# Performance work log

Hardware: AMD Instinct MI355X
Metric: run time of the kernel (lower is better)

The kernel has to match this reference:

```python
import jax, jax.numpy as jnp
import numpy as np

N_NODES = 100000
N_EDGES = 1600000
IN_DIM = 128
OUT_DIM = 64


def setup_inputs() -> dict:
    key = jax.random.key(0)
    k1, k2, k3 = jax.random.split(key, 3)
    x = jax.random.normal(k1, (N_NODES, IN_DIM), dtype=jnp.float32)
    edge_index = jax.random.randint(k2, (2, N_EDGES), 0, N_NODES, dtype=jnp.int64)
    W = jax.random.normal(k3, (IN_DIM, OUT_DIM), dtype=jnp.float32) * (1.0 / np.sqrt(IN_DIM))
    b = jnp.zeros((OUT_DIM,), dtype=jnp.float32)
    return {"x": x, "edge_index": edge_index, "W": W, "b": b}


def reference(x, edge_index, W, b):
    row = edge_index[0]  # source nodes
    col = edge_index[1]  # target nodes (aggregation index)
    n = x.shape[0]

    # gcn_norm with add_self_loops=False: degree from edge weights (ones) at target
    ones = jnp.ones((edge_index.shape[1],), dtype=x.dtype)
    deg = jax.ops.segment_sum(ones, col, num_segments=n)  # [N]
    deg_inv_sqrt = jnp.where(deg > 0, jax.lax.rsqrt(jnp.maximum(deg, 1e-12)), 0.0)
    norm = deg_inv_sqrt[row] * deg_inv_sqrt[col]  # [E]

    # linear transform first (bias added after aggregation, as in PyG GCNConv)
    h = x @ W  # [N, OUT_DIM]

    # gather source features, scale by norm, scatter-add to targets
    msg = h[row] * norm[:, None]  # [E, OUT_DIM]
    out = jax.ops.segment_sum(msg, col, num_segments=n) + b  # [N, OUT_DIM]

    return jax.nn.relu(out)
```

## Files before the change

kernel.cpp:

```cpp
#include <hip/hip_runtime.h>
#include <hip/hip_bf16.h>

#define IN_DIM 128
#define OUT_DIM 64
#define FLOG 7
#define FNPB (1 << FLOG)
#define MAXFINE 1024
#define BB 512
#define BT 512
#define MAXE 8
#define NGRP 8
#define CAP_G 512
#define CAP (NGRP * CAP_G)
#define SPILL_MAX 65536
#define KFT 256
#define HALF 64
#define SBUF_CAP 2048

static inline size_t align_up(size_t v, size_t a) { return (v + a - 1) & ~(a - 1); }

__device__ __forceinline__ unsigned short f2bf(float f) {
    unsigned int x = __float_as_uint(f);
    unsigned int r = (x + 0x7fffu + ((x >> 16) & 1u)) >> 16;
    return (unsigned short)r;
}

typedef _Float16 half8 __attribute__((ext_vector_type(8)));
typedef float f32x4 __attribute__((ext_vector_type(4)));

__global__ void __launch_bounds__(BT, 4) k_build_mm(
    const int* __restrict__ row, const int* __restrict__ col,
    int* __restrict__ BinSize, unsigned int* __restrict__ EdgeBuf,
    uint2* __restrict__ spill, int* __restrict__ spillcur,
    const float* __restrict__ x, const float* __restrict__ W,
    unsigned short* __restrict__ h,
    int n_edges, int n_nodes, int nbf, int chunk, int mm_blocks) {
    if ((int)blockIdx.x < BB) {
        __shared__ int hist[MAXFINE];
        int t = threadIdx.x;
        int g = blockIdx.x & (NGRP - 1);
        int start = blockIdx.x * chunk;
        int end = min(n_edges, start + chunk);
        int n = end - start;

        for (int i = t; i < nbf; i += BT) hist[i] = 0;
        __syncthreads();

        int er[MAXE], ec[MAXE];
#pragma unroll
        for (int u = 0; u < MAXE; ++u) {
            int i = t + u * BT;
            ec[u] = -1;
            if (i < n) {
                er[u] = row[start + i];
                int c = col[start + i];
                ec[u] = c;
                atomicAdd(&hist[c >> FLOG], 1);
            }
        }
        __syncthreads();
        for (int i = t; i < nbf; i += BT) {
            int cv = hist[i];
            hist[i] = cv ? atomicAdd(&BinSize[g * nbf + i], cv) : 0;
        }
        __syncthreads();
#pragma unroll
        for (int u = 0; u < MAXE; ++u) {
            int c = ec[u];
            if (c >= 0) {
                int bin = c >> FLOG;
                int pos = atomicAdd(&hist[bin], 1);
                if (pos < CAP_G) {
                    EdgeBuf[(size_t)bin * CAP + g * CAP_G + pos] =
                        ((unsigned int)er[u] << FLOG) | (unsigned int)(c & (FNPB - 1));
                } else {
                    int sp = atomicAdd(spillcur, 1);
                    if (sp < SPILL_MAX)
                        spill[sp] = make_uint2((unsigned int)er[u], (unsigned int)c);
                }
            }
        }
    } else {
        const int lane = threadIdx.x & 63;
        const int m = lane & 15;
        const int q = lane >> 4;
        const int wv = threadIdx.x >> 6;
        const int wid0 = ((int)blockIdx.x - BB) * 8 + wv;
        const int nwaves = mm_blocks * 8;
        const int ntiles = (n_nodes + 15) >> 4;

        half8 bfrag[4][4];
#pragma unroll
        for (int kt = 0; kt < 4; ++kt) {
#pragma unroll
            for (int nt = 0; nt < 4; ++nt) {
                int k0 = kt * 32 + q * 8;
                int c = nt * 16 + m;
#pragma unroll
                for (int j = 0; j < 8; ++j)
                    bfrag[kt][nt][j] = (_Float16)W[(size_t)(k0 + j) * OUT_DIM + c];
            }
        }

        for (int wid = wid0; wid < ntiles; wid += nwaves) {
            const int nb = wid << 4;
            int arow = nb + m;
            if (arow >= n_nodes) arow = n_nodes - 1;
            const float* xr = x + (size_t)arow * IN_DIM;

            f32x4 acc[4];
#pragma unroll
            for (int nt = 0; nt < 4; ++nt) acc[nt] = (f32x4){0.f, 0.f, 0.f, 0.f};

#pragma unroll
            for (int kt = 0; kt < 4; ++kt) {
                const float4* xp = (const float4*)(xr + kt * 32 + q * 8);
                float4 lo = xp[0];
                float4 hi = xp[1];
                half8 afrag;
                afrag[0] = (_Float16)lo.x; afrag[1] = (_Float16)lo.y;
                afrag[2] = (_Float16)lo.z; afrag[3] = (_Float16)lo.w;
                afrag[4] = (_Float16)hi.x; afrag[5] = (_Float16)hi.y;
                afrag[6] = (_Float16)hi.z; afrag[7] = (_Float16)hi.w;
#pragma unroll
                for (int nt = 0; nt < 4; ++nt)
                    acc[nt] = __builtin_amdgcn_mfma_f32_16x16x32_f16(
                        afrag, bfrag[kt][nt], acc[nt], 0, 0, 0);
            }

#pragma unroll
            for (int r = 0; r < 4; ++r) {
                int node = nb + q * 4 + r;
                if (node < n_nodes) {
                    unsigned short* hp = h + (size_t)node * OUT_DIM + m;
#pragma unroll
                    for (int nt = 0; nt < 4; ++nt)
                        hp[nt * 16] = f2bf(acc[nt][r]);
                }
            }
        }
    }
}

__global__ void __launch_bounds__(256) kD_degree(
    const unsigned int* __restrict__ EdgeBuf, const int* __restrict__ BinSize,
    const uint2* __restrict__ spill, const int* __restrict__ spillcur,
    float* __restrict__ dis, int* __restrict__ cntg, int n_nodes, int nbf) {
    __shared__ int cnt[FNPB];
    int t = threadIdx.x;
    int b = blockIdx.x;
    if (t < FNPB) cnt[t] = 0;
    __syncthreads();
    for (int g = 0; g < NGRP; ++g) {
        int szg = min(BinSize[g * nbf + b], CAP_G);
        const unsigned int* sl = EdgeBuf + (size_t)b * CAP + g * CAP_G;
        for (int i = t; i < szg; i += 256)
            atomicAdd(&cnt[sl[i] & (FNPB - 1)], 1);
    }
    int sn = min(*spillcur, SPILL_MAX);
    for (int i = t; i < sn; i += 256) {
        uint2 e = spill[i];
        if ((int)(e.y >> FLOG) == b) atomicAdd(&cnt[e.y & (FNPB - 1)], 1);
    }
    __syncthreads();
    if (t < FNPB) {
        int d = cnt[t];
        cntg[(size_t)b * FNPB + t] = d;
        int node = (b << FLOG) + t;
        if (node < n_nodes)
            dis[node] = (d > 0) ? rsqrtf((float)d) : 0.0f;
    }
}

__global__ void __launch_bounds__(KFT) kF_sortagg(
    const unsigned int* __restrict__ EdgeBuf, const int* __restrict__ BinSize,
    const uint2* __restrict__ spill, const int* __restrict__ spillcur,
    const unsigned short* __restrict__ h, const float* __restrict__ dis,
    const int* __restrict__ cntg, const float* __restrict__ b,
    float* __restrict__ out, int* __restrict__ arena, int* __restrict__ arenacur,
    int n_nodes, int nbf) {
    __shared__ int cnt[HALF];
    __shared__ int seg[HALF];
    __shared__ int cursor[HALF];
    __shared__ int sbuf[SBUF_CAP];
    __shared__ int abase_sh;
    int t = threadIdx.x;
    int bk = blockIdx.x >> 1;
    int halfid = blockIdx.x & 1;
    int lo = halfid * HALF;
    int nb0 = (bk << FLOG) + lo;
    int sn = min(*spillcur, SPILL_MAX);

    if (t < 64) {
        int c = cntg[(size_t)bk * FNPB + lo + t];
        int s = c;
#pragma unroll
        for (int off = 1; off < 64; off <<= 1) {
            int y = __shfl_up(s, off, 64);
            if (t >= off) s += y;
        }
        cnt[t] = c;
        seg[t] = s;
        cursor[t] = s - c;
    }
    __syncthreads();

    int ne = seg[HALF - 1];
    if (t == 0 && ne > SBUF_CAP) abase_sh = atomicAdd(arenacur, ne);
    __syncthreads();

    const int lane = t & 63;
    const int wv = t >> 6;
    const int quarter = lane >> 4;
    const int qlane = lane & 15;
    float4 bias = ((const float4*)b)[qlane];

    if (ne <= SBUF_CAP) {
        for (int g = 0; g < NGRP; ++g) {
            int szg = min(BinSize[g * nbf + bk], CAP_G);
            const unsigned int* sl = EdgeBuf + (size_t)bk * CAP + g * CAP_G;
            for (int i = t; i < szg; i += KFT) {
                unsigned int v = sl[i];
                int nlocal = (int)(v & (FNPB - 1)) - lo;
                if ((unsigned)nlocal < HALF) {
                    int p = atomicAdd(&cursor[nlocal], 1);
                    sbuf[p] = (int)(v >> FLOG);
                }
            }
        }
        for (int i = t; i < sn; i += KFT) {
            uint2 e = spill[i];
            if ((int)(e.y >> FLOG) == bk) {
                int nlocal = (int)(e.y & (FNPB - 1)) - lo;
                if ((unsigned)nlocal < HALF) {
                    int p = atomicAdd(&cursor[nlocal], 1);
                    sbuf[p] = (int)e.x;
                }
            }
        }
        __syncthreads();

        for (int nl = wv; nl < HALF; nl += 4) {
            int node = nb0 + nl;
            if (node >= n_nodes) break;
            int e_ = seg[nl];
            int dcount = cnt[nl];
            int s_ = e_ - dcount;
            float a0 = 0.f, a1 = 0.f, a2 = 0.f, a3 = 0.f;
            for (int j0 = s_; j0 < e_; j0 += 16) {
                int i0 = j0 + quarter;
                int i1 = i0 + 4;
                int i2 = i0 + 8;
                int i3 = i0 + 12;
                int r0 = sbuf[i0 < e_ ? i0 : s_];
                int r1 = sbuf[i1 < e_ ? i1 : s_];
                int r2 = sbuf[i2 < e_ ? i2 : s_];
                int r3 = sbuf[i3 < e_ ? i3 : s_];
                float d0 = dis[r0];
                float d1 = dis[r1];
                float d2 = dis[r2];
                float d3 = dis[r3];
                uint2 v0 = make_uint2(0u, 0u), v1 = v0, v2 = v0, v3 = v0;
                if (i0 < e_)
                    v0 = *(const uint2*)(h + (size_t)r0 * OUT_DIM + qlane * 4);
                if (i1 < e_)
                    v1 = *(const uint2*)(h + (size_t)r1 * OUT_DIM + qlane * 4);
                if (i2 < e_)
                    v2 = *(const uint2*)(h + (size_t)r2 * OUT_DIM + qlane * 4);
                if (i3 < e_)
                    v3 = *(const uint2*)(h + (size_t)r3 * OUT_DIM + qlane * 4);
                a0 = fmaf(__uint_as_float(v0.x << 16), d0, a0);
                a1 = fmaf(__uint_as_float(v0.x & 0xFFFF0000u), d0, a1);
                a2 = fmaf(__uint_as_float(v0.y << 16), d0, a2);
                a3 = fmaf(__uint_as_float(v0.y & 0xFFFF0000u), d0, a3);
                a0 = fmaf(__uint_as_float(v1.x << 16), d1, a0);
                a1 = fmaf(__uint_as_float(v1.x & 0xFFFF0000u), d1, a1);
                a2 = fmaf(__uint_as_float(v1.y << 16), d1, a2);
                a3 = fmaf(__uint_as_float(v1.y & 0xFFFF0000u), d1, a3);
                a0 = fmaf(__uint_as_float(v2.x << 16), d2, a0);
                a1 = fmaf(__uint_as_float(v2.x & 0xFFFF0000u), d2, a1);
                a2 = fmaf(__uint_as_float(v2.y << 16), d2, a2);
                a3 = fmaf(__uint_as_float(v2.y & 0xFFFF0000u), d2, a3);
                a0 = fmaf(__uint_as_float(v3.x << 16), d3, a0);
                a1 = fmaf(__uint_as_float(v3.x & 0xFFFF0000u), d3, a1);
                a2 = fmaf(__uint_as_float(v3.y << 16), d3, a2);
                a3 = fmaf(__uint_as_float(v3.y & 0xFFFF0000u), d3, a3);
            }
            a0 += __shfl_xor(a0, 16, 64); a0 += __shfl_xor(a0, 32, 64);
            a1 += __shfl_xor(a1, 16, 64); a1 += __shfl_xor(a1, 32, 64);
            a2 += __shfl_xor(a2, 16, 64); a2 += __shfl_xor(a2, 32, 64);
            a3 += __shfl_xor(a3, 16, 64); a3 += __shfl_xor(a3, 32, 64);
            if (quarter == 0) {
                float dv = (dcount > 0) ? rsqrtf((float)dcount) : 0.0f;
                float4 o;
                o.x = fmaxf(fmaf(a0, dv, bias.x), 0.f);
                o.y = fmaxf(fmaf(a1, dv, bias.y), 0.f);
                o.z = fmaxf(fmaf(a2, dv, bias.z), 0.f);
                o.w = fmaxf(fmaf(a3, dv, bias.w), 0.f);
                ((float4*)(out + (size_t)node * OUT_DIM))[qlane] = o;
            }
        }
    } else {
        int abase = abase_sh;
        for (int g = 0; g < NGRP; ++g) {
            int szg = min(BinSize[g * nbf + bk], CAP_G);
            const unsigned int* sl = EdgeBuf + (size_t)bk * CAP + g * CAP_G;
            for (int i = t; i < szg; i += KFT) {
                unsigned int v = sl[i];
                int nlocal = (int)(v & (FNPB - 1)) - lo;
                if ((unsigned)nlocal < HALF) {
                    int p = atomicAdd(&cursor[nlocal], 1);
                    arena[abase + p] = (int)(v >> FLOG);
                }
            }
        }
        for (int i = t; i < sn; i += KFT) {
            uint2 e = spill[i];
            if ((int)(e.y >> FLOG) == bk) {
                int nlocal = (int)(e.y & (FNPB - 1)) - lo;
                if ((unsigned)nlocal < HALF) {
                    int p = atomicAdd(&cursor[nlocal], 1);
                    arena[abase + p] = (int)e.x;
                }
            }
        }
        __threadfence();
        __syncthreads();
        for (int nl = wv; nl < HALF; nl += 4) {
            int node = nb0 + nl;
            if (node >= n_nodes) break;
            int e_ = seg[nl];
            int dcount = cnt[nl];
            int s_ = e_ - dcount;
            float a0 = 0.f, a1 = 0.f, a2 = 0.f, a3 = 0.f;
            for (int j0 = s_; j0 < e_; j0 += 8) {
                int iA = j0 + quarter;
                int iB = j0 + quarter + 4;
                int rA = arena[abase + (iA < e_ ? iA : s_)];
                int rB = arena[abase + (iB < e_ ? iB : s_)];
                float dA = dis[rA];
                float dB = dis[rB];
                uint2 vA = make_uint2(0u, 0u), vB = make_uint2(0u, 0u);
                if (iA < e_)
                    vA = *(const uint2*)(h + (size_t)rA * OUT_DIM + qlane * 4);
                if (iB < e_)
                    vB = *(const uint2*)(h + (size_t)rB * OUT_DIM + qlane * 4);
                a0 = fmaf(__uint_as_float(vA.x << 16), dA, a0);
                a1 = fmaf(__uint_as_float(vA.x & 0xFFFF0000u), dA, a1);
                a2 = fmaf(__uint_as_float(vA.y << 16), dA, a2);
                a3 = fmaf(__uint_as_float(vA.y & 0xFFFF0000u), dA, a3);
                a0 = fmaf(__uint_as_float(vB.x << 16), dB, a0);
                a1 = fmaf(__uint_as_float(vB.x & 0xFFFF0000u), dB, a1);
                a2 = fmaf(__uint_as_float(vB.y << 16), dB, a2);
                a3 = fmaf(__uint_as_float(vB.y & 0xFFFF0000u), dB, a3);
            }
            a0 += __shfl_xor(a0, 16, 64); a0 += __shfl_xor(a0, 32, 64);
            a1 += __shfl_xor(a1, 16, 64); a1 += __shfl_xor(a1, 32, 64);
            a2 += __shfl_xor(a2, 16, 64); a2 += __shfl_xor(a2, 32, 64);
            a3 += __shfl_xor(a3, 16, 64); a3 += __shfl_xor(a3, 32, 64);
            if (quarter == 0) {
                float dv = (dcount > 0) ? rsqrtf((float)dcount) : 0.0f;
                float4 o;
                o.x = fmaxf(fmaf(a0, dv, bias.x), 0.f);
                o.y = fmaxf(fmaf(a1, dv, bias.y), 0.f);
                o.z = fmaxf(fmaf(a2, dv, bias.z), 0.f);
                o.w = fmaxf(fmaf(a3, dv, bias.w), 0.f);
                ((float4*)(out + (size_t)node * OUT_DIM))[qlane] = o;
            }
        }
    }
}

#define MM_NODES 16
__global__ void __launch_bounds__(256) k_matmul_f32(
    const float* __restrict__ x, const float* __restrict__ W,
    const float* __restrict__ dis, float* __restrict__ h, int n_nodes) {
    __shared__ float xs[MM_NODES * IN_DIM];
    const int lane = threadIdx.x & 63;
    const int wv = threadIdx.x >> 6;
    float w[IN_DIM];
#pragma unroll
    for (int k = 0; k < IN_DIM; ++k) w[k] = W[k * OUT_DIM + lane];
    int nchunks = (n_nodes + MM_NODES - 1) / MM_NODES;
    for (int ch = blockIdx.x; ch < nchunks; ch += gridDim.x) {
        int base = ch * MM_NODES;
        int nrows = min(MM_NODES, n_nodes - base);
        __syncthreads();
        const float4* xg = (const float4*)(x + (size_t)base * IN_DIM);
        int nf4 = nrows * IN_DIM / 4;
        for (int i = threadIdx.x; i < nf4; i += 256) ((float4*)xs)[i] = xg[i];
        __syncthreads();
#pragma unroll
        for (int j = 0; j < 4; ++j) {
            int local = wv * 4 + j;
            int node = base + local;
            if (local < nrows) {
                const float4* xr = (const float4*)(xs + local * IN_DIM);
                float acc = 0.0f;
#pragma unroll
                for (int k4 = 0; k4 < IN_DIM / 4; ++k4) {
                    float4 xv = xr[k4];
                    acc = fmaf(xv.x, w[k4 * 4 + 0], acc);
                    acc = fmaf(xv.y, w[k4 * 4 + 1], acc);
                    acc = fmaf(xv.z, w[k4 * 4 + 2], acc);
                    acc = fmaf(xv.w, w[k4 * 4 + 3], acc);
                }
                h[(size_t)node * OUT_DIM + lane] = acc * dis[node];
            }
        }
    }
}

__global__ void k_degree_fb(const int* __restrict__ col, int* __restrict__ deg,
                            int n_edges) {
    int i = blockIdx.x * blockDim.x + threadIdx.x;
    int stride = gridDim.x * blockDim.x;
    for (; i < n_edges; i += stride) atomicAdd(&deg[col[i]], 1);
}

__global__ void k_rsqrt_fb(const int* __restrict__ deg, float* __restrict__ dis, int n) {
    int i = blockIdx.x * blockDim.x + threadIdx.x;
    if (i < n) {
        int d = deg[i];
        dis[i] = (d > 0) ? rsqrtf((float)d) : 0.0f;
    }
}

__global__ void __launch_bounds__(256) k_scatter_fb(
    const int* __restrict__ row, const int* __restrict__ col,
    const float* __restrict__ dis, const float* __restrict__ h,
    float* __restrict__ out, int n_edges) {
    const int lane = threadIdx.x & 63;
    int e = (blockIdx.x * blockDim.x + threadIdx.x) >> 6;
    int nw = (gridDim.x * blockDim.x) >> 6;
    for (; e < n_edges; e += nw) {
        int r = row[e];
        int c = col[e];
        float v = h[(size_t)r * OUT_DIM + lane] * dis[c];
        atomicAdd(&out[(size_t)c * OUT_DIM + lane], v);
    }
}

__global__ void k_bias_relu_fb(float* __restrict__ out, const float* __restrict__ b,
                               int total) {
    int i = blockIdx.x * blockDim.x + threadIdx.x;
    int stride = gridDim.x * blockDim.x;
    for (; i < total; i += stride) {
        float v = out[i] + b[i & (OUT_DIM - 1)];
        out[i] = fmaxf(v, 0.0f);
    }
}

extern "C" void kernel_launch(void* const* d_in, const int* in_sizes, int n_in,
                              void* d_out, int out_size, void* d_ws, size_t ws_size,
                              hipStream_t stream) {
    const float* x = (const float*)d_in[0];
    const int* ei = (const int*)d_in[1];
    const float* W = (const float*)d_in[2];
    const float* b = (const float*)d_in[3];
    float* out = (float*)d_out;

    const int n_nodes = in_sizes[0] / IN_DIM;
    const int n_edges = in_sizes[1] / 2;
    const int* row = ei;
    const int* col = ei + n_edges;

    const int nbf = (n_nodes + FNPB - 1) >> FLOG;
    const int chunk = (n_edges + BB - 1) / BB;

    char* wsb = (char*)d_ws;
    size_t off = 0;
    int* BinSize = (int*)(wsb + off);    off += (size_t)(nbf * NGRP + 8) * 4;
    int* spillcur = BinSize + nbf * NGRP;
    int* arenacur = BinSize + nbf * NGRP + 1;
    const size_t zero_bytes = off;
    off = align_up(off, 256);
    unsigned int* EdgeBuf = (unsigned int*)(wsb + off);
                                         off += align_up((size_t)nbf * CAP * 4, 256);
    uint2* spill = (uint2*)(wsb + off);  off += align_up((size_t)SPILL_MAX * 8, 256);
    int* arena = (int*)(wsb + off);      off += align_up((size_t)n_edges * 4, 256);
    float* dis = (float*)(wsb + off);    off += align_up((size_t)n_nodes * 4, 256);
    int* cntg = (int*)(wsb + off);       off += align_up((size_t)nbf * FNPB * 4, 256);
    unsigned short* h = (unsigned short*)(wsb + off);
                                         off += (size_t)n_nodes * OUT_DIM * 2;
    const size_t needed = off;

    const bool ok = (ws_size >= needed) && (nbf <= MAXFINE) &&
                    (chunk <= MAXE * BT) && (n_nodes <= (1 << 24));

    if (ok) {
        const int ntiles = (n_nodes + 15) >> 4;
        int mm_blocks = (ntiles + 15) / 16;
        if (mm_blocks < 1) mm_blocks = 1;
        hipMemsetAsync(BinSize, 0, zero_bytes, stream);
        k_build_mm<<<BB + mm_blocks, BT, 0, stream>>>(
            row, col, BinSize, EdgeBuf, spill, spillcur,
            x, W, h, n_edges, n_nodes, nbf, chunk, mm_blocks);
        kD_degree<<<nbf, 256, 0, stream>>>(EdgeBuf, BinSize, spill, spillcur,
                                           dis, cntg, n_nodes, nbf);
        kF_sortagg<<<2 * nbf, KFT, 0, stream>>>(EdgeBuf, BinSize, spill, spillcur,
                                                h, dis, cntg, b, out, arena,
                                                arenacur, n_nodes, nbf);
    } else {
        char* p = (char*)d_ws;
        int* deg_f = (int*)p;
        float* dis_f = (float*)(p + align_up((size_t)n_nodes * 4, 256));
        float* h_f = (float*)(p + 2 * align_up((size_t)n_nodes * 4, 256));
        hipMemsetAsync(deg_f, 0, (size_t)n_nodes * 4, stream);
        hipMemsetAsync(out, 0, (size_t)out_size * 4, stream);
        k_degree_fb<<<1024, 256, 0, stream>>>(col, deg_f, n_edges);
        k_rsqrt_fb<<<(n_nodes + 255) / 256, 256, 0, stream>>>(deg_f, dis_f, n_nodes);
        k_matmul_f32<<<1024, 256, 0, stream>>>(x, W, dis_f, h_f, n_nodes);
        k_scatter_fb<<<2048, 256, 0, stream>>>(row, col, dis_f, h_f, out, n_edges);
        k_bias_relu_fb<<<2048, 256, 0, stream>>>(out, b, n_nodes * OUT_DIM);
    }
}
```

Before: 172.2 us.

## Stage edges in LDS by bin before coalesced writes to global edge buffer

The edge-binning phase now uses 128 larger blocks, each holding 12544 edges. Each block builds a histogram, runs a prefix scan to lay the edges out contiguously by bin in shared memory, then has one wave per bin write runs to EdgeBuf so the stores are coalesced instead of scattered one by one. This cuts global scatter traffic and atomic contention, but it needs about 62KB of LDS per block. That LDS is also declared in the matmul blocks, and launch bounds drop to 2, so occupancy for the fused matmul path falls and there are fewer binning blocks to run in parallel.

```diff
diff --git a/kernel.cpp b/kernel.cpp
--- a/kernel.cpp
+++ b/kernel.cpp
@@ -6,9 +6,9 @@
 #define FLOG 7
 #define FNPB (1 << FLOG)
 #define MAXFINE 1024
-#define BB 512
+#define BB 128
 #define BT 512
-#define MAXE 8
+#define EPB 12544
 #define NGRP 8
 #define CAP_G 512
 #define CAP (NGRP * CAP_G)
@@ -28,55 +28,89 @@
 typedef _Float16 half8 __attribute__((ext_vector_type(8)));
 typedef float f32x4 __attribute__((ext_vector_type(4)));
 
-__global__ void __launch_bounds__(BT, 4) k_build_mm(
+__global__ void __launch_bounds__(BT, 2) k_build_mm(
     const int* __restrict__ row, const int* __restrict__ col,
     int* __restrict__ BinSize, unsigned int* __restrict__ EdgeBuf,
     uint2* __restrict__ spill, int* __restrict__ spillcur,
     const float* __restrict__ x, const float* __restrict__ W,
     unsigned short* __restrict__ h,
     int n_edges, int n_nodes, int nbf, int chunk, int mm_blocks) {
+    __shared__ int hist[MAXFINE];
+    __shared__ int cursor[MAXFINE];
+    __shared__ int gdelta[MAXFINE];
+    __shared__ int wtot[8];
+    __shared__ unsigned int sped[EPB];
     if ((int)blockIdx.x < BB) {
-        __shared__ int hist[MAXFINE];
         int t = threadIdx.x;
         int g = blockIdx.x & (NGRP - 1);
         int start = blockIdx.x * chunk;
         int end = min(n_edges, start + chunk);
         int n = end - start;
 
-        for (int i = t; i < nbf; i += BT) hist[i] = 0;
-        __syncthreads();
-
-        int er[MAXE], ec[MAXE];
-#pragma unroll
-        for (int u = 0; u < MAXE; ++u) {
-            int i = t + u * BT;
-            ec[u] = -1;
-            if (i < n) {
-                er[u] = row[start + i];
-                int c = col[start + i];
-                ec[u] = c;
-                atomicAdd(&hist[c >> FLOG], 1);
-            }
-        }
-        __syncthreads();
-        for (int i = t; i < nbf; i += BT) {
-            int cv = hist[i];
-            hist[i] = cv ? atomicAdd(&BinSize[g * nbf + i], cv) : 0;
-        }
-        __syncthreads();
-#pragma unroll
-        for (int u = 0; u < MAXE; ++u) {
-            int c = ec[u];
-            if (c >= 0) {
-                int bin = c >> FLOG;
-                int pos = atomicAdd(&hist[bin], 1);
-                if (pos < CAP_G) {
-                    EdgeBuf[(size_t)bin * CAP + g * CAP_G + pos] =
-                        ((unsigned int)er[u] << FLOG) | (unsigned int)(c & (FNPB - 1));
-                } else {
-                    int sp = atomicAdd(spillcur, 1);
-                    if (sp < SPILL_MAX)
-                        spill[sp] = make_uint2((unsigned int)er[u], (unsigned int)c);
+        for (int i = t; i < MAXFINE; i += BT) hist[i] = 0;
+        __syncthreads();
+
+        for (int i = t; i < n; i += BT) {
+            int c = col[start + i];
+            atomicAdd(&hist[c >> FLOG], 1);
+        }
+        __syncthreads();
+
+        {
+            int b0 = 2 * t, b1 = 2 * t + 1;
+            int c0 = hist[b0], c1 = hist[b1];
+            int s = c0 + c1;
+            int lane = t & 63, wv = t >> 6;
+#pragma unroll
+            for (int off = 1; off < 64; off <<= 1) {
+                int y = __shfl_up(s, off, 64);
+                if (lane >= off) s += y;
+            }
+            if (lane == 63) wtot[wv] = s;
+            __syncthreads();
+            int woff = 0;
+            for (int w = 0; w < wv; ++w) woff += wtot[w];
+            int incl = woff + s;
+            int l1 = incl - c1;
+            int l0 = l1 - c0;
+            cursor[b0] = l0;
+            cursor[b1] = l1;
+            int g0 = c0 ? atomicAdd(&BinSize[g * nbf + b0], c0) : 0;
+            int g1 = c1 ? atomicAdd(&BinSize[g * nbf + b1], c1) : 0;
+            gdelta[b0] = g0;
+            gdelta[b1] = g1;
+        }
+        __syncthreads();
+
+        for (int i = t; i < n; i += BT) {
+            int r = row[start + i];
+            int c = col[start + i];
+            int bin = c >> FLOG;
+            int p = atomicAdd(&cursor[bin], 1);
+            sped[p] = ((unsigned int)r << FLOG) | (unsigned int)(c & (FNPB - 1));
+        }
+        __syncthreads();
+
+        {
+            int lane = t & 63, wv = t >> 6;
+            for (int b = wv; b < nbf; b += 8) {
+                int cnt = hist[b];
+                if (!cnt) continue;
+                int lst = cursor[b] - cnt;
+                int goff = gdelta[b];
+                unsigned int* dst = EdgeBuf + (size_t)b * CAP + g * CAP_G;
+                for (int k = lane; k < cnt; k += 64) {
+                    unsigned int v = sped[lst + k];
+                    int off = goff + k;
+                    if (off < CAP_G) {
+                        dst[off] = v;
+                    } else {
+                        int sp = atomicAdd(spillcur, 1);
+                        if (sp < SPILL_MAX)
+                            spill[sp] = make_uint2(
+                                v >> FLOG,
+                                ((unsigned int)b << FLOG) | (v & (FNPB - 1)));
+                    }
                 }
             }
         }
@@ -486,7 +520,7 @@
     const size_t needed = off;
 
     const bool ok = (ws_size >= needed) && (nbf <= MAXFINE) &&
-                    (chunk <= MAXE * BT) && (n_nodes <= (1 << 24));
+                    (chunk <= EPB) && (n_nodes <= (1 << 24));
 
     if (ok) {
         const int ntiles = (n_nodes + 15) >> 4;
```

Result: no change. 174.5 us (+1.3%).
